# Kernel tuning notes

Measured on AMD Instinct MI355X. Metric: run time of the kernel, lower is better.

The kernel has to match this reference:

```python
import jax, jax.numpy as jnp
import numpy as np

BS, C, H, W = 4, 128, 64, 64  # input_dim=128
INNER = 64


def setup_inputs() -> dict:
    key = jax.random.key(0)
    ks = jax.random.split(key, 9)
    s_in = 1.0 / np.sqrt(C)
    s_inner = 1.0 / np.sqrt(INNER)
    return {
        "inpt": jax.random.normal(ks[0], (BS, C, H, W), dtype=jnp.float32),
        "Wq": jax.random.normal(ks[1], (INNER, C), dtype=jnp.float32) * s_in,
        "bq": jax.random.normal(ks[2], (INNER,), dtype=jnp.float32) * 0.01,
        "Wk": jax.random.normal(ks[3], (INNER, C), dtype=jnp.float32) * s_in,
        "bk": jax.random.normal(ks[4], (INNER,), dtype=jnp.float32) * 0.01,
        "Wv": jax.random.normal(ks[5], (INNER, C), dtype=jnp.float32) * s_in,
        "bv": jax.random.normal(ks[6], (INNER,), dtype=jnp.float32) * 0.01,
        "Wo": jax.random.normal(ks[7], (C, INNER), dtype=jnp.float32) * s_inner,
        "bo": jax.random.normal(ks[8], (C,), dtype=jnp.float32) * 0.01,
    }


def reference(inpt, Wq, bq, Wk, bk, Wv, bv, Wo, bo):
    bs, c, h, w = inpt.shape
    L = h * w
    # [bs, C, H, W] -> [bs, L, C] (tokens = spatial positions)
    x = inpt.reshape(bs, c, L).transpose(0, 2, 1)
    q = jnp.einsum('blc,dc->bld', x, Wq) + bq  # [bs, L, INNER]
    k = jnp.einsum('blc,dc->bld', x, Wk) + bk
    v = jnp.einsum('blc,dc->bld', x, Wv) + bv
    # torch code divides by np.round(sqrt(d), 2); for d=64 this is exactly 8.0
    scale = jnp.float32(np.round(np.sqrt(q.shape[-1]), 2))
    scores = jnp.einsum('bld,bmd->blm', q, k) / scale  # [bs, L, L] score matrix
    factors = jax.nn.softmax(scores, axis=-1)
    ctx = jnp.einsum('blm,bmd->bld', factors, v)  # [bs, L, INNER]
    out = jnp.einsum('bld,cd->blc', ctx, Wo) + bo  # [bs, L, C]
    out = out.transpose(0, 2, 1).reshape(bs, c, h, w)
    return inpt + out
```

## Files before the change

### kernel.cpp

```cpp
#include <hip/hip_runtime.h>
#include <hip/hip_bf16.h>

typedef __bf16 bf16x8 __attribute__((ext_vector_type(8)));
typedef __bf16 bf16x4 __attribute__((ext_vector_type(4)));
typedef short  s16x4  __attribute__((ext_vector_type(4)));
typedef float  f32x4  __attribute__((ext_vector_type(4)));

#define MFMA32(a, b, c) __builtin_amdgcn_mfma_f32_16x16x32_bf16((a), (b), (c), 0, 0, 0)
#define MFMA16K(a, b, c) __builtin_amdgcn_mfma_f32_16x16x16bf16_1k((a), (b), (c), 0, 0, 0)

#if __has_builtin(__builtin_amdgcn_exp2f)
#define EXP2F(x) __builtin_amdgcn_exp2f(x)
#else
#define EXP2F(x) __expf(0.6931471805599453f * (x))
#endif

#define GL16(G, L)                                                            \
    __builtin_amdgcn_global_load_lds(                                         \
        (const __attribute__((address_space(1))) void*)(G),                   \
        (__attribute__((address_space(3))) void*)(L), 16, 0, 0)

#define SPLIT 4
#define QSCALE 0.18033688011112042f
#define BBOUND 12.0f


__global__ __launch_bounds__(256) void qkv_kernel(
    const float* __restrict__ inpt,
    const float* __restrict__ Wq, const float* __restrict__ bq,
    const float* __restrict__ Wk, const float* __restrict__ bk,
    const float* __restrict__ Wv, const float* __restrict__ bv,
    __bf16* __restrict__ Qws, __bf16* __restrict__ Kws, __bf16* __restrict__ VTws)
{
    __shared__ __align__(16) __bf16 xT[16 * 140];
    __shared__ __align__(16) __bf16 os[16 * 144];
    const int bid = blockIdx.x;
    const int b   = bid >> 8;
    const int l0  = (bid & 255) << 4;
    const int t   = threadIdx.x;

    {
        const int c = t >> 1, half = t & 1;
        const float* xin = inpt + ((size_t)(b * 128 + c)) * 4096 + l0 + half * 8;
        float4 v0 = *(const float4*)xin;
        float4 v1 = *(const float4*)(xin + 4);
        const int tok0 = half * 8;
        xT[(tok0 + 0) * 140 + c] = (__bf16)v0.x;
        xT[(tok0 + 1) * 140 + c] = (__bf16)v0.y;
        xT[(tok0 + 2) * 140 + c] = (__bf16)v0.z;
        xT[(tok0 + 3) * 140 + c] = (__bf16)v0.w;
        xT[(tok0 + 4) * 140 + c] = (__bf16)v1.x;
        xT[(tok0 + 5) * 140 + c] = (__bf16)v1.y;
        xT[(tok0 + 6) * 140 + c] = (__bf16)v1.z;
        xT[(tok0 + 7) * 140 + c] = (__bf16)v1.w;
    }
    __syncthreads();

    const int w    = t >> 6;
    const int lane = t & 63;
    const int quad = lane >> 4;
    const int l15  = lane & 15;

    f32x4 acc[3];
    #pragma unroll
    for (int j = 0; j < 3; ++j)
        #pragma unroll
        for (int r = 0; r < 4; ++r) acc[j][r] = 0.f;

    #pragma unroll
    for (int ks = 0; ks < 4; ++ks) {
        bf16x8 af = *(const bf16x8*)&xT[l15 * 140 + ks * 32 + quad * 8];
        #pragma unroll
        for (int j = 0; j < 3; ++j) {
            const int wn   = w * 3 + j;
            const int msel = wn >> 2;
            const float* W = (msel == 0) ? Wq : ((msel == 1) ? Wk : Wv);
            const float* Wp = W + ((wn & 3) * 16 + l15) * 128 + ks * 32 + quad * 8;
            float4 wa = *(const float4*)Wp;
            float4 wb = *(const float4*)(Wp + 4);
            bf16x8 bf;
            bf[0] = (__bf16)wa.x; bf[1] = (__bf16)wa.y;
            bf[2] = (__bf16)wa.z; bf[3] = (__bf16)wa.w;
            bf[4] = (__bf16)wb.x; bf[5] = (__bf16)wb.y;
            bf[6] = (__bf16)wb.z; bf[7] = (__bf16)wb.w;
            acc[j] = MFMA32(af, bf, acc[j]);
        }
    }

    #pragma unroll
    for (int j = 0; j < 3; ++j) {
        const int wn   = w * 3 + j;
        const int msel = wn >> 2;
        const int o0   = (wn & 3) * 16;
        const float* bb = (msel == 0) ? bq : ((msel == 1) ? bk : bv);
        float bias = bb[o0 + l15];
        if (msel < 2) {
            const float scl = (msel == 0) ? QSCALE : 1.0f;
            const int oc = wn * 16 + l15;
            #pragma unroll
            for (int r = 0; r < 4; ++r)
                os[(quad * 4 + r) * 144 + oc] = (__bf16)((acc[j][r] + bias) * scl);
        } else {
            const int d  = o0 + l15;
            const int kt = l0 >> 6;
            const int kc = (l0 >> 4) & 3;
            bf16x4 v;
            #pragma unroll
            for (int r = 0; r < 4; ++r) v[r] = (__bf16)(acc[j][r] + bias);
            *(bf16x4*)(VTws + (size_t)b * 262144 + kt * 4096
                       + d * 64 + quad * 16 + kc * 4) = v;
        }
    }
    __syncthreads();

    {
        const int tok = t >> 4, c = t & 15;
        bf16x8 v = *(const bf16x8*)&os[tok * 144 + c * 8];
        if (c < 8) {
            *(bf16x8*)(Qws + ((size_t)(b * 4096 + l0 + tok)) * 64 + c * 8) = v;
        } else {
            const int d8 = c - 8;
            __bf16* dst = Kws + (size_t)b * 262144
                + (l0 >> 6) * 4096
                + ((l0 >> 4) & 3) * 1024
                + (d8 >> 2) * 512
                + (d8 & 3) * 128
                + tok * 8;
            *(bf16x8*)dst = v;
        }
    }
}

__global__ __launch_bounds__(256, 4) void attn_kernel(
    const __bf16* __restrict__ Qws, const __bf16* __restrict__ Kws,
    const __bf16* __restrict__ VTws,
    __bf16* __restrict__ Ops, float* __restrict__ Lws)
{
    __shared__ __align__(16) __bf16 sbuf[2][4096];

    const int bid   = blockIdx.x;
    const int split = bid >> 8;
    const int qt    = bid & 255;
    const int b  = qt >> 6;
    const int l0 = (qt & 63) << 6;
    const int t    = threadIdx.x;
    const int w    = t >> 6;
    const int lane = t & 63;
    const int quad = lane >> 4;
    const int l15  = lane & 15;

    const __bf16* qptr = Qws + ((size_t)(b * 4096 + l0 + w * 16 + l15)) * 64 + quad * 8;
    bf16x8 qf0 = *(const bf16x8*)qptr;
    bf16x8 qf1 = *(const bf16x8*)(qptr + 32);

    f32x4 cfr[4];
    #pragma unroll
    for (int mt = 0; mt < 4; ++mt)
        #pragma unroll
        for (int r = 0; r < 4; ++r) cfr[mt][r] = 0.f;
    float l_run = 0.f;

    int voff[8];
    #pragma unroll
    for (int mt = 0; mt < 4; ++mt) {
        const int d = mt * 16 + l15;
        #pragma unroll
        for (int kc8 = 0; kc8 < 2; ++kc8)
            voff[kc8 * 4 + mt] = d * 64 + (((2 * quad + kc8) ^ (d & 7)) * 8);
    }

    const uint4* Vg = (const uint4*)(VTws + ((size_t)b << 18));
    const int rw = t >> 3, cw = (t & 7) ^ ((t >> 3) & 7);
    const uint4* vp = Vg + rw * 8 + cw + split * 8192;

    const __bf16* Kgl = Kws + ((size_t)b << 18)
                      + (size_t)(split * 16) * 4096 + lane * 8;

    union B4 { bf16x4 h; s16x4 s; };
    union V8 { bf16x8 v; s16x4 q[2]; };

    auto stageV = [&](__bf16* Bb) {
        GL16(vp,       Bb +        w * 512);
        GL16(vp + 256, Bb + 2048 + w * 512);
        vp += 512;
    };

    bf16x8 kfA[4][2], kfB[4][2];
    auto loadK = [&](bf16x8 (*kf)[2], int kt) {
        const __bf16* p = Kgl + (size_t)kt * 4096;
        #pragma unroll
        for (int nt = 0; nt < 4; ++nt) {
            kf[nt][0] = *(const bf16x8*)(p + nt * 1024);
            kf[nt][1] = *(const bf16x8*)(p + nt * 1024 + 512);
        }
    };

    auto tile_step = [&](const __bf16* __restrict__ B, bf16x8 (*kf)[2]) {
        B4 pk[4];
        float ps[4];
        #pragma unroll
        for (int nt = 0; nt < 4; ++nt) {
            f32x4 a = {-BBOUND, -BBOUND, -BBOUND, -BBOUND};
            a = MFMA32(kf[nt][0], qf0, a);
            a = MFMA32(kf[nt][1], qf1, a);
            float p0 = EXP2F(a[0]), p1 = EXP2F(a[1]);
            float p2 = EXP2F(a[2]), p3 = EXP2F(a[3]);
            pk[nt].h[0] = (__bf16)p0; pk[nt].h[1] = (__bf16)p1;
            pk[nt].h[2] = (__bf16)p2; pk[nt].h[3] = (__bf16)p3;
            ps[nt] = (p0 + p1) + (p2 + p3);
        }
        float psum = (ps[0] + ps[1]) + (ps[2] + ps[3]);
        psum += __shfl_xor(psum, 16);
        psum += __shfl_xor(psum, 32);
        l_run += psum;

        #pragma unroll
        for (int kc8 = 0; kc8 < 2; ++kc8) {
            #pragma unroll
            for (int mt = 0; mt < 4; ++mt) {
                V8 vv;
                vv.v = *(const bf16x8*)&B[voff[kc8 * 4 + mt]];
                cfr[mt] = MFMA16K(vv.q[0], pk[2 * kc8 + 0].s, cfr[mt]);
                cfr[mt] = MFMA16K(vv.q[1], pk[2 * kc8 + 1].s, cfr[mt]);
            }
        }
    };

    stageV(sbuf[0]);
    loadK(kfA, 0);

    for (int kt2 = 0; kt2 < 8; ++kt2) {
        __syncthreads();
        stageV(sbuf[1]);
        loadK(kfB, 2 * kt2 + 1);
        tile_step(sbuf[0], kfA);
        __syncthreads();
        if (kt2 < 7) {
            stageV(sbuf[0]);
            loadK(kfA, 2 * kt2 + 2);
        }
        tile_step(sbuf[1], kfB);
    }
    __syncthreads();

    {
        __bf16* tb = (__bf16*)sbuf + w * 1088;
        #pragma unroll
        for (int mt = 0; mt < 4; ++mt) {
            bf16x4 v;
            #pragma unroll
            for (int r = 0; r < 4; ++r) v[r] = (__bf16)cfr[mt][r];
            *(bf16x4*)&tb[l15 * 68 + mt * 16 + quad * 4] = v;
        }
        const int rowbase = (split * 4 + b) * 4096 + l0 + w * 16;
        #pragma unroll
        for (int h = 0; h < 2; ++h) {
            const int chunk = lane + h * 64;
            const int tok = chunk >> 3, c8 = chunk & 7;
            bf16x8 v = *(const bf16x8*)&tb[tok * 68 + c8 * 8];
            *(bf16x8*)(Ops + (size_t)(rowbase + tok) * 64 + c8 * 8) = v;
        }
        if (quad == 0) Lws[rowbase + l15] = l_run;
    }
}

__global__ __launch_bounds__(256) void outproj_kernel(
    const float* __restrict__ inpt,
    const __bf16* __restrict__ Ops, const float* __restrict__ Lws,
    const float* __restrict__ Wo, const float* __restrict__ bo,
    float* __restrict__ out)
{
    __shared__ __align__(16) __bf16 cx[16 * 72];
    const int bid = blockIdx.x;
    const int b   = bid >> 8;
    const int l0  = (bid & 255) << 4;
    const int t   = threadIdx.x;

    {
        const int token = t >> 4, d4 = (t & 15) << 2;
        const int rowb  = b * 4096 + l0 + token;
        float denom = 0.f;
        #pragma unroll
        for (int s = 0; s < SPLIT; ++s) denom += Lws[s * 16384 + rowb];
        const float inv = 1.f / denom;
        float ax = 0.f, ay = 0.f, az = 0.f, aw = 0.f;
        #pragma unroll
        for (int s = 0; s < SPLIT; ++s) {
            const bf16x4 v = *(const bf16x4*)(Ops
                + ((size_t)(s * 16384 + rowb)) * 64 + d4);
            ax += (float)v[0]; ay += (float)v[1];
            az += (float)v[2]; aw += (float)v[3];
        }
        bf16x4 pv;
        pv[0] = (__bf16)(ax * inv); pv[1] = (__bf16)(ay * inv);
        pv[2] = (__bf16)(az * inv); pv[3] = (__bf16)(aw * inv);
        *(bf16x4*)&cx[token * 72 + d4] = pv;
    }
    __syncthreads();

    const int w    = t >> 6;
    const int lane = t & 63;
    const int quad = lane >> 4;
    const int l15  = lane & 15;

    f32x4 acc[2];
    #pragma unroll
    for (int mi = 0; mi < 2; ++mi)
        #pragma unroll
        for (int r = 0; r < 4; ++r) acc[mi][r] = 0.f;

    #pragma unroll
    for (int ks = 0; ks < 2; ++ks) {
        bf16x8 bfrag = *(const bf16x8*)&cx[l15 * 72 + ks * 32 + quad * 8];
        #pragma unroll
        for (int mi = 0; mi < 2; ++mi) {
            const int crow = (w * 2 + mi) * 16 + l15;
            const float* Wp = Wo + crow * 64 + ks * 32 + quad * 8;
            float4 wa = *(const float4*)Wp;
            float4 wb = *(const float4*)(Wp + 4);
            bf16x8 afrag;
            afrag[0] = (__bf16)wa.x; afrag[1] = (__bf16)wa.y;
            afrag[2] = (__bf16)wa.z; afrag[3] = (__bf16)wa.w;
            afrag[4] = (__bf16)wb.x; afrag[5] = (__bf16)wb.y;
            afrag[6] = (__bf16)wb.z; afrag[7] = (__bf16)wb.w;
            acc[mi] = MFMA32(afrag, bfrag, acc[mi]);
        }
    }

    #pragma unroll
    for (int mi = 0; mi < 2; ++mi) {
        #pragma unroll
        for (int r = 0; r < 4; ++r) {
            const int c = (w * 2 + mi) * 16 + quad * 4 + r;
            const size_t addr = ((size_t)(b * 128 + c)) * 4096 + l0 + l15;
            out[addr] = inpt[addr] + bo[c] + acc[mi][r];
        }
    }
}

extern "C" void kernel_launch(void* const* d_in, const int* in_sizes, int n_in,
                              void* d_out, int out_size, void* d_ws, size_t ws_size,
                              hipStream_t stream)
{
    const float* inpt = (const float*)d_in[0];
    const float* Wq   = (const float*)d_in[1];
    const float* bq   = (const float*)d_in[2];
    const float* Wk   = (const float*)d_in[3];
    const float* bk   = (const float*)d_in[4];
    const float* Wv   = (const float*)d_in[5];
    const float* bv   = (const float*)d_in[6];
    const float* Wo   = (const float*)d_in[7];
    const float* bo   = (const float*)d_in[8];
    float* out = (float*)d_out;

    char* ws = (char*)d_ws;
    const size_t MB = (size_t)1 << 20;
    __bf16* Qws  = (__bf16*)(ws + 0 * MB);
    __bf16* Kws  = (__bf16*)(ws + 2 * MB);
    __bf16* VTws = (__bf16*)(ws + 4 * MB);
    __bf16* Ops  = (__bf16*)(ws + 6 * MB);
    float*  Lws  = (float*)(ws + 16 * MB);

    qkv_kernel<<<1024, 256, 0, stream>>>(inpt, Wq, bq, Wk, bk, Wv, bv, Qws, Kws, VTws);
    attn_kernel<<<SPLIT * 256, 256, 0, stream>>>(Qws, Kws, VTws, Ops, Lws);
    outproj_kernel<<<1024, 256, 0, stream>>>(inpt, Ops, Lws, Wo, bo, out);
}
```

Before: 125.2 us.

## Load V fragments straight from global into registers, dropping LDS staging

The attention kernel no longer stages each V tile into double-buffered shared memory with async global-to-LDS copies. Each wave now reads its V MFMA fragments directly from global memory into registers, and the per-tile __syncthreads barriers are removed. Launch bounds are relaxed from 4 to 3 blocks per CU to leave room for the extra vector registers. The goal is to cut barrier stalls and LDS traffic. The cost is that all four waves redundantly fetch the same V tile through the cache, and occupancy may drop.

```diff
diff --git a/kernel.cpp b/kernel.cpp
--- a/kernel.cpp
+++ b/kernel.cpp
@@ -14,11 +14,6 @@
 #else
 #define EXP2F(x) __expf(0.6931471805599453f * (x))
 #endif
-
-#define GL16(G, L)                                                            \
-    __builtin_amdgcn_global_load_lds(                                         \
-        (const __attribute__((address_space(1))) void*)(G),                   \
-        (__attribute__((address_space(3))) void*)(L), 16, 0, 0)
 
 #define SPLIT 4
 #define QSCALE 0.18033688011112042f
@@ -131,12 +126,12 @@
     }
 }
 
-__global__ __launch_bounds__(256, 4) void attn_kernel(
+__global__ __launch_bounds__(256, 3) void attn_kernel(
     const __bf16* __restrict__ Qws, const __bf16* __restrict__ Kws,
     const __bf16* __restrict__ VTws,
     __bf16* __restrict__ Ops, float* __restrict__ Lws)
 {
-    __shared__ __align__(16) __bf16 sbuf[2][4096];
+    __shared__ __align__(16) __bf16 tbuf[4 * 1088];
 
     const int bid   = blockIdx.x;
     const int split = bid >> 8;
@@ -160,30 +155,13 @@
         for (int r = 0; r < 4; ++r) cfr[mt][r] = 0.f;
     float l_run = 0.f;
 
-    int voff[8];
-    #pragma unroll
-    for (int mt = 0; mt < 4; ++mt) {
-        const int d = mt * 16 + l15;
-        #pragma unroll
-        for (int kc8 = 0; kc8 < 2; ++kc8)
-            voff[kc8 * 4 + mt] = d * 64 + (((2 * quad + kc8) ^ (d & 7)) * 8);
-    }
-
-    const uint4* Vg = (const uint4*)(VTws + ((size_t)b << 18));
-    const int rw = t >> 3, cw = (t & 7) ^ ((t >> 3) & 7);
-    const uint4* vp = Vg + rw * 8 + cw + split * 8192;
-
     const __bf16* Kgl = Kws + ((size_t)b << 18)
                       + (size_t)(split * 16) * 4096 + lane * 8;
+    const __bf16* Vgl = VTws + ((size_t)b << 18)
+                      + (size_t)(split * 16) * 4096 + l15 * 64 + quad * 16;
 
     union B4 { bf16x4 h; s16x4 s; };
     union V8 { bf16x8 v; s16x4 q[2]; };
-
-    auto stageV = [&](__bf16* Bb) {
-        GL16(vp,       Bb +        w * 512);
-        GL16(vp + 256, Bb + 2048 + w * 512);
-        vp += 512;
-    };
 
     bf16x8 kfA[4][2], kfB[4][2];
     auto loadK = [&](bf16x8 (*kf)[2], int kt) {
@@ -195,7 +173,15 @@
         }
     };
 
-    auto tile_step = [&](const __bf16* __restrict__ B, bf16x8 (*kf)[2]) {
+    auto tile_step = [&](int kt, bf16x8 (*kf)[2]) {
+        const __bf16* vp = Vgl + (size_t)kt * 4096;
+        V8 vv[2][4];
+        #pragma unroll
+        for (int kc8 = 0; kc8 < 2; ++kc8)
+            #pragma unroll
+            for (int mt = 0; mt < 4; ++mt)
+                vv[kc8][mt].v = *(const bf16x8*)(vp + mt * 1024 + kc8 * 8);
+
         B4 pk[4];
         float ps[4];
         #pragma unroll
@@ -218,33 +204,22 @@
         for (int kc8 = 0; kc8 < 2; ++kc8) {
             #pragma unroll
             for (int mt = 0; mt < 4; ++mt) {
-                V8 vv;
-                vv.v = *(const bf16x8*)&B[voff[kc8 * 4 + mt]];
-                cfr[mt] = MFMA16K(vv.q[0], pk[2 * kc8 + 0].s, cfr[mt]);
-                cfr[mt] = MFMA16K(vv.q[1], pk[2 * kc8 + 1].s, cfr[mt]);
+                cfr[mt] = MFMA16K(vv[kc8][mt].q[0], pk[2 * kc8 + 0].s, cfr[mt]);
+                cfr[mt] = MFMA16K(vv[kc8][mt].q[1], pk[2 * kc8 + 1].s, cfr[mt]);
             }
         }
     };
 
-    stageV(sbuf[0]);
     loadK(kfA, 0);
-
     for (int kt2 = 0; kt2 < 8; ++kt2) {
-        __syncthreads();
-        stageV(sbuf[1]);
         loadK(kfB, 2 * kt2 + 1);
-        tile_step(sbuf[0], kfA);
-        __syncthreads();
-        if (kt2 < 7) {
-            stageV(sbuf[0]);
-            loadK(kfA, 2 * kt2 + 2);
-        }
-        tile_step(sbuf[1], kfB);
-    }
-    __syncthreads();
+        tile_step(2 * kt2, kfA);
+        if (kt2 < 7) loadK(kfA, 2 * kt2 + 2);
+        tile_step(2 * kt2 + 1, kfB);
+    }
 
     {
-        __bf16* tb = (__bf16*)sbuf + w * 1088;
+        __bf16* tb = tbuf + w * 1088;
         #pragma unroll
         for (int mt = 0; mt < 4; ++mt) {
             bf16x4 v;
```

Result: slower. 172.2 us (+37.5%).

## Triple-buffer V tiles in LDS with partial vmcnt waits before barriers

Applied to the files above, without the earlier changes.

The attention loop now uses three LDS slots for V instead of two and prefetches V two tiles ahead. Each full __syncthreads is replaced by a manual s_waitcnt vmcnt(10) plus s_barrier, so later V and K loads can stay in flight across the barrier. The aim is to hide global-to-LDS latency and shorten barrier stalls. In exchange it uses 50% more shared memory per block and relies on a hand-counted vmcnt that must match the exact load issue order.

```diff
diff --git a/kernel.cpp b/kernel.cpp
--- a/kernel.cpp
+++ b/kernel.cpp
@@ -136,7 +136,7 @@
     const __bf16* __restrict__ VTws,
     __bf16* __restrict__ Ops, float* __restrict__ Lws)
 {
-    __shared__ __align__(16) __bf16 sbuf[2][4096];
+    __shared__ __align__(16) __bf16 sbuf[3][4096];
 
     const int bid   = blockIdx.x;
     const int split = bid >> 8;
@@ -171,7 +171,7 @@
 
     const uint4* Vg = (const uint4*)(VTws + ((size_t)b << 18));
     const int rw = t >> 3, cw = (t & 7) ^ ((t >> 3) & 7);
-    const uint4* vp = Vg + rw * 8 + cw + split * 8192;
+    const uint4* vbase = Vg + rw * 8 + cw + split * 8192;
 
     const __bf16* Kgl = Kws + ((size_t)b << 18)
                       + (size_t)(split * 16) * 4096 + lane * 8;
@@ -179,10 +179,11 @@
     union B4 { bf16x4 h; s16x4 s; };
     union V8 { bf16x8 v; s16x4 q[2]; };
 
-    auto stageV = [&](__bf16* Bb) {
+    auto stageV = [&](int kt, int slot) {
+        __bf16* Bb = &sbuf[slot][0];
+        const uint4* vp = vbase + (size_t)kt * 512;
         GL16(vp,       Bb +        w * 512);
         GL16(vp + 256, Bb + 2048 + w * 512);
-        vp += 512;
     };
 
     bf16x8 kfA[4][2], kfB[4][2];
@@ -226,22 +227,37 @@
         }
     };
 
-    stageV(sbuf[0]);
+#define WAITBAR()                                                             \
+    do {                                                                      \
+        asm volatile("s_waitcnt vmcnt(10)" ::: "memory");                     \
+        __builtin_amdgcn_s_barrier();                                         \
+        asm volatile("" ::: "memory");                                        \
+    } while (0)
+
+    stageV(0, 0);
+    stageV(1, 1);
     loadK(kfA, 0);
 
+    int cons = 0;
+    int stg  = 2;
     for (int kt2 = 0; kt2 < 8; ++kt2) {
-        __syncthreads();
-        stageV(sbuf[1]);
-        loadK(kfB, 2 * kt2 + 1);
-        tile_step(sbuf[0], kfA);
-        __syncthreads();
-        if (kt2 < 7) {
-            stageV(sbuf[0]);
-            loadK(kfA, 2 * kt2 + 2);
-        }
-        tile_step(sbuf[1], kfB);
-    }
-    __syncthreads();
+        const int h0 = 2 * kt2;
+        WAITBAR();
+        if (kt2 < 7) stageV(h0 + 2, stg);
+        loadK(kfB, h0 + 1);
+        tile_step(&sbuf[cons][0], kfA);
+        cons = (cons == 2) ? 0 : cons + 1;
+        stg  = (stg  == 2) ? 0 : stg  + 1;
+        WAITBAR();
+        if (kt2 < 7) { stageV(h0 + 3, stg); loadK(kfA, h0 + 2); }
+        tile_step(&sbuf[cons][0], kfB);
+        cons = (cons == 2) ? 0 : cons + 1;
+        stg  = (stg  == 2) ? 0 : stg  + 1;
+    }
+#undef WAITBAR
+
+    __builtin_amdgcn_s_barrier();
+    asm volatile("" ::: "memory");
 
     {
         __bf16* tb = (__bf16*)sbuf + w * 1088;
```

After: 125.5 us. No clear change (+0.3%).

## Double query tile per block, stage K in LDS, and split keys eightfold

Applied to the files above, without the earlier changes.

Each attention block now handles 128 queries (two 16-row subtiles per wave) over 512 keys. The key split grows from 4 to 8, which keeps the same number of blocks. K is now staged through LDS with global_load_lds next to V, where before each wave loaded it from global into registers. Each K and V fragment read from LDS now feeds two query subtiles, which halves shared-memory and global traffic per FLOP. s_setprio is raised around the PV MFMA section. In exchange the kernel uses more registers and twice the LDS, and writes twice as many partial rows to Ops, which the output projection then has to reduce.

```diff
diff --git a/kernel.cpp b/kernel.cpp
--- a/kernel.cpp
+++ b/kernel.cpp
@@ -20,7 +20,7 @@
         (const __attribute__((address_space(1))) void*)(G),                   \
         (__attribute__((address_space(3))) void*)(L), 16, 0, 0)
 
-#define SPLIT 4
+#define SPLIT 8
 #define QSCALE 0.18033688011112042f
 #define BBOUND 12.0f
 
@@ -136,29 +136,36 @@
     const __bf16* __restrict__ VTws,
     __bf16* __restrict__ Ops, float* __restrict__ Lws)
 {
-    __shared__ __align__(16) __bf16 sbuf[2][4096];
+    __shared__ __align__(16) __bf16 sbuf[2][8192];
 
     const int bid   = blockIdx.x;
-    const int split = bid >> 8;
-    const int qt    = bid & 255;
-    const int b  = qt >> 6;
-    const int l0 = (qt & 63) << 6;
+    const int split = bid >> 7;
+    const int qi    = bid & 127;
+    const int b  = qi >> 5;
+    const int l0 = (qi & 31) << 7;
     const int t    = threadIdx.x;
     const int w    = t >> 6;
     const int lane = t & 63;
     const int quad = lane >> 4;
     const int l15  = lane & 15;
 
-    const __bf16* qptr = Qws + ((size_t)(b * 4096 + l0 + w * 16 + l15)) * 64 + quad * 8;
-    bf16x8 qf0 = *(const bf16x8*)qptr;
-    bf16x8 qf1 = *(const bf16x8*)(qptr + 32);
-
-    f32x4 cfr[4];
-    #pragma unroll
-    for (int mt = 0; mt < 4; ++mt)
-        #pragma unroll
-        for (int r = 0; r < 4; ++r) cfr[mt][r] = 0.f;
-    float l_run = 0.f;
+    bf16x8 qf[2][2];
+    #pragma unroll
+    for (int qs = 0; qs < 2; ++qs) {
+        const __bf16* qptr = Qws
+            + ((size_t)(b * 4096 + l0 + w * 32 + qs * 16 + l15)) * 64 + quad * 8;
+        qf[qs][0] = *(const bf16x8*)qptr;
+        qf[qs][1] = *(const bf16x8*)(qptr + 32);
+    }
+
+    f32x4 cfr[2][4];
+    #pragma unroll
+    for (int qs = 0; qs < 2; ++qs)
+        #pragma unroll
+        for (int mt = 0; mt < 4; ++mt)
+            #pragma unroll
+            for (int r = 0; r < 4; ++r) cfr[qs][mt][r] = 0.f;
+    float l_acc[2] = {0.f, 0.f};
 
     int voff[8];
     #pragma unroll
@@ -171,96 +178,99 @@
 
     const uint4* Vg = (const uint4*)(VTws + ((size_t)b << 18));
     const int rw = t >> 3, cw = (t & 7) ^ ((t >> 3) & 7);
-    const uint4* vp = Vg + rw * 8 + cw + split * 8192;
-
-    const __bf16* Kgl = Kws + ((size_t)b << 18)
-                      + (size_t)(split * 16) * 4096 + lane * 8;
+    const uint4* vbase = Vg + rw * 8 + cw + split * 4096;
+    const uint4* kbase = (const uint4*)(Kws + ((size_t)b << 18))
+                       + t + split * 4096;
 
     union B4 { bf16x4 h; s16x4 s; };
     union V8 { bf16x8 v; s16x4 q[2]; };
 
-    auto stageV = [&](__bf16* Bb) {
-        GL16(vp,       Bb +        w * 512);
-        GL16(vp + 256, Bb + 2048 + w * 512);
-        vp += 512;
+    auto stage = [&](int kt, int slot) {
+        __bf16* Kd = &sbuf[slot][0];
+        __bf16* Vd = &sbuf[slot][4096];
+        const uint4* kp = kbase + kt * 512;
+        const uint4* vp = vbase + kt * 512;
+        GL16(kp,       Kd +        w * 512);
+        GL16(kp + 256, Kd + 2048 + w * 512);
+        GL16(vp,       Vd +        w * 512);
+        GL16(vp + 256, Vd + 2048 + w * 512);
     };
 
-    bf16x8 kfA[4][2], kfB[4][2];
-    auto loadK = [&](bf16x8 (*kf)[2], int kt) {
-        const __bf16* p = Kgl + (size_t)kt * 4096;
+    auto tile_step = [&](int slot) {
+        const __bf16* Kb = &sbuf[slot][0];
+        const __bf16* Vb = &sbuf[slot][4096];
+        B4 pk[2][4];
         #pragma unroll
         for (int nt = 0; nt < 4; ++nt) {
-            kf[nt][0] = *(const bf16x8*)(p + nt * 1024);
-            kf[nt][1] = *(const bf16x8*)(p + nt * 1024 + 512);
-        }
-    };
-
-    auto tile_step = [&](const __bf16* __restrict__ B, bf16x8 (*kf)[2]) {
-        B4 pk[4];
-        float ps[4];
-        #pragma unroll
-        for (int nt = 0; nt < 4; ++nt) {
-            f32x4 a = {-BBOUND, -BBOUND, -BBOUND, -BBOUND};
-            a = MFMA32(kf[nt][0], qf0, a);
-            a = MFMA32(kf[nt][1], qf1, a);
-            float p0 = EXP2F(a[0]), p1 = EXP2F(a[1]);
-            float p2 = EXP2F(a[2]), p3 = EXP2F(a[3]);
-            pk[nt].h[0] = (__bf16)p0; pk[nt].h[1] = (__bf16)p1;
-            pk[nt].h[2] = (__bf16)p2; pk[nt].h[3] = (__bf16)p3;
-            ps[nt] = (p0 + p1) + (p2 + p3);
-        }
-        float psum = (ps[0] + ps[1]) + (ps[2] + ps[3]);
-        psum += __shfl_xor(psum, 16);
-        psum += __shfl_xor(psum, 32);
-        l_run += psum;
-
+            bf16x8 k0 = *(const bf16x8*)(Kb + nt * 1024 +       lane * 8);
+            bf16x8 k1 = *(const bf16x8*)(Kb + nt * 1024 + 512 + lane * 8);
+            #pragma unroll
+            for (int qs = 0; qs < 2; ++qs) {
+                f32x4 a = {-BBOUND, -BBOUND, -BBOUND, -BBOUND};
+                a = MFMA32(k0, qf[qs][0], a);
+                a = MFMA32(k1, qf[qs][1], a);
+                float p0 = EXP2F(a[0]), p1 = EXP2F(a[1]);
+                float p2 = EXP2F(a[2]), p3 = EXP2F(a[3]);
+                pk[qs][nt].h[0] = (__bf16)p0; pk[qs][nt].h[1] = (__bf16)p1;
+                pk[qs][nt].h[2] = (__bf16)p2; pk[qs][nt].h[3] = (__bf16)p3;
+                l_acc[qs] += (p0 + p1) + (p2 + p3);
+            }
+        }
+        __builtin_amdgcn_s_setprio(1);
         #pragma unroll
         for (int kc8 = 0; kc8 < 2; ++kc8) {
             #pragma unroll
             for (int mt = 0; mt < 4; ++mt) {
                 V8 vv;
-                vv.v = *(const bf16x8*)&B[voff[kc8 * 4 + mt]];
-                cfr[mt] = MFMA16K(vv.q[0], pk[2 * kc8 + 0].s, cfr[mt]);
-                cfr[mt] = MFMA16K(vv.q[1], pk[2 * kc8 + 1].s, cfr[mt]);
+                vv.v = *(const bf16x8*)&Vb[voff[kc8 * 4 + mt]];
+                #pragma unroll
+                for (int qs = 0; qs < 2; ++qs) {
+                    cfr[qs][mt] = MFMA16K(vv.q[0], pk[qs][2 * kc8 + 0].s, cfr[qs][mt]);
+                    cfr[qs][mt] = MFMA16K(vv.q[1], pk[qs][2 * kc8 + 1].s, cfr[qs][mt]);
+                }
             }
         }
+        __builtin_amdgcn_s_setprio(0);
     };
 
-    stageV(sbuf[0]);
-    loadK(kfA, 0);
-
-    for (int kt2 = 0; kt2 < 8; ++kt2) {
-        __syncthreads();
-        stageV(sbuf[1]);
-        loadK(kfB, 2 * kt2 + 1);
-        tile_step(sbuf[0], kfA);
-        __syncthreads();
-        if (kt2 < 7) {
-            stageV(sbuf[0]);
-            loadK(kfA, 2 * kt2 + 2);
-        }
-        tile_step(sbuf[1], kfB);
-    }
-    __syncthreads();
+    stage(0, 0);
+    for (int h = 0; h < 8; ++h) {
+        asm volatile("s_waitcnt vmcnt(0)" ::: "memory");
+        __builtin_amdgcn_s_barrier();
+        asm volatile("" ::: "memory");
+        if (h < 7) stage(h + 1, (h + 1) & 1);
+        tile_step(h & 1);
+    }
+
+    __builtin_amdgcn_s_barrier();
+    asm volatile("" ::: "memory");
 
     {
-        __bf16* tb = (__bf16*)sbuf + w * 1088;
-        #pragma unroll
-        for (int mt = 0; mt < 4; ++mt) {
-            bf16x4 v;
-            #pragma unroll
-            for (int r = 0; r < 4; ++r) v[r] = (__bf16)cfr[mt][r];
-            *(bf16x4*)&tb[l15 * 68 + mt * 16 + quad * 4] = v;
-        }
-        const int rowbase = (split * 4 + b) * 4096 + l0 + w * 16;
-        #pragma unroll
-        for (int h = 0; h < 2; ++h) {
-            const int chunk = lane + h * 64;
+        __bf16* tb = (__bf16*)sbuf + w * 2176;
+        #pragma unroll
+        for (int qs = 0; qs < 2; ++qs)
+            #pragma unroll
+            for (int mt = 0; mt < 4; ++mt) {
+                bf16x4 v;
+                #pragma unroll
+                for (int r = 0; r < 4; ++r) v[r] = (__bf16)cfr[qs][mt][r];
+                *(bf16x4*)&tb[(qs * 16 + l15) * 68 + mt * 16 + quad * 4] = v;
+            }
+        const int rowbase = (split * 4 + b) * 4096 + l0 + w * 32;
+        #pragma unroll
+        for (int hh = 0; hh < 4; ++hh) {
+            const int chunk = lane + hh * 64;
             const int tok = chunk >> 3, c8 = chunk & 7;
             bf16x8 v = *(const bf16x8*)&tb[tok * 68 + c8 * 8];
             *(bf16x8*)(Ops + (size_t)(rowbase + tok) * 64 + c8 * 8) = v;
         }
-        if (quad == 0) Lws[rowbase + l15] = l_run;
+        #pragma unroll
+        for (int qs = 0; qs < 2; ++qs) {
+            float lr = l_acc[qs];
+            lr += __shfl_xor(lr, 16);
+            lr += __shfl_xor(lr, 32);
+            if (quad == 0) Lws[rowbase + qs * 16 + l15] = lr;
+        }
     }
 }
 
@@ -359,9 +369,9 @@
     __bf16* Kws  = (__bf16*)(ws + 2 * MB);
     __bf16* VTws = (__bf16*)(ws + 4 * MB);
     __bf16* Ops  = (__bf16*)(ws + 6 * MB);
-    float*  Lws  = (float*)(ws + 16 * MB);
+    float*  Lws  = (float*)(ws + 24 * MB);
 
     qkv_kernel<<<1024, 256, 0, stream>>>(inpt, Wq, bq, Wk, bk, Wv, bv, Qws, Kws, VTws);
-    attn_kernel<<<SPLIT * 256, 256, 0, stream>>>(Qws, Kws, VTws, Ops, Lws);
+    attn_kernel<<<SPLIT * 128, 256, 0, stream>>>(Qws, Kws, VTws, Ops, Lws);
     outproj_kernel<<<1024, 256, 0, stream>>>(inpt, Ops, Lws, Wo, bo, out);
 }
```

Measured after the change: 125.0 us. Within noise of the previous version (-0.2%).
